# Kernel optimization log

Hardware: AMD Instinct MI355X
Metric: run time of the kernel (lower is better)

Reference implementation:

```python
import jax, jax.numpy as jnp
import numpy as np

N_NODES = 100000


def gcn_conv(x, edge_index, W, b, n_nodes):
    # PyG GCNConv: add self-loops, symmetric normalization D^-1/2 (A+I) D^-1/2, then XW + b
    xw = x @ W  # [N, out]
    loops = jnp.arange(n_nodes, dtype=edge_index.dtype)
    src = jnp.concatenate([edge_index[0], loops])  # [E+N]
    dst = jnp.concatenate([edge_index[1], loops])
    deg = jax.ops.segment_sum(jnp.ones_like(dst, dtype=xw.dtype), dst, num_segments=n_nodes)
    dinv = jnp.where(deg > 0, deg ** -0.5, 0.0).astype(xw.dtype)
    norm = dinv[src] * dinv[dst]  # [E+N]
    msgs = xw[src] * norm[:, None]  # gather source features, scale
    out = jax.ops.segment_sum(msgs, dst, num_segments=n_nodes)  # scatter-add at dst
    return out + b


def setup_inputs() -> dict:
    key = jax.random.key(0)
    k1, k2, k3, k4 = jax.random.split(key, 4)
    F_in, dim, n_cls, n_edges = 512, 32, 40, 3200000
    x = jax.random.normal(k1, (N_NODES, F_in), dtype=jnp.float32)
    edge_index = jax.random.randint(k2, (2, n_edges), 0, N_NODES, dtype=jnp.int64)
    W1 = jax.random.normal(k3, (F_in, dim), dtype=jnp.float32) * (1.0 / np.sqrt(F_in))
    b1 = jnp.zeros((dim,), dtype=jnp.float32)
    W2 = jax.random.normal(k4, (dim, n_cls), dtype=jnp.float32) * (1.0 / np.sqrt(dim))
    b2 = jnp.zeros((n_cls,), dtype=jnp.float32)
    return {"x": x, "edge_index": edge_index, "W1": W1, "b1": b1, "W2": W2, "b2": b2}


def reference(x, edge_index, W1, b1, W2, b2):
    h = jax.nn.relu(gcn_conv(x, edge_index, W1, b1, N_NODES))
    # F.dropout with training=False (eval) is identity
    logits = gcn_conv(h, edge_index, W2, b2, N_NODES)
    return jax.nn.log_softmax(logits, axis=1)
```

## Files before the change

kernel.cpp:

```cpp
#include <hip/hip_runtime.h>
#include <math.h>


#define DIM 32
#define NCLS 40
#define F_IN 512
#define BSH 8
#define EPB 8192
#define LMAX 9216

__device__ __forceinline__ unsigned int bf16rne(float x) {
    unsigned int u = __float_as_uint(x);
    return (u + 0x7fffu + ((u >> 16) & 1u)) >> 16;
}
__device__ __forceinline__ unsigned int packpair(float lo, float hi) {
    return bf16rne(lo) | (bf16rne(hi) << 16);
}
__device__ __forceinline__ void unpack8(uint4 u, float* f) {
    f[0] = __uint_as_float(u.x << 16);
    f[1] = __uint_as_float(u.x & 0xffff0000u);
    f[2] = __uint_as_float(u.y << 16);
    f[3] = __uint_as_float(u.y & 0xffff0000u);
    f[4] = __uint_as_float(u.z << 16);
    f[5] = __uint_as_float(u.z & 0xffff0000u);
    f[6] = __uint_as_float(u.w << 16);
    f[7] = __uint_as_float(u.w & 0xffff0000u);
}

__global__ __launch_bounds__(256) void initcur_k(int* __restrict__ gcur) {
    int t = blockIdx.x * 256 + threadIdx.x;
    if (t < 512) gcur[t] = t * LMAX;
}

__global__ __launch_bounds__(256) void part_k(const int* __restrict__ src,
                                              const int* __restrict__ dst,
                                              int* __restrict__ gcur,
                                              int* __restrict__ pairs, int E) {
    __shared__ int st[EPB];
    __shared__ int h[512];
    __shared__ int hb[512];
    int tid = threadIdx.x;
    h[tid] = 0; h[tid + 256] = 0;
    __syncthreads();
    int base = blockIdx.x * EPB;
#pragma unroll 4
    for (int k = 0; k < EPB / 256; ++k) {
        int e = base + k * 256 + tid;
        if (e < E) {
            int d = dst[e];
            st[k * 256 + tid] = d;
            atomicAdd(&h[d >> BSH], 1);
        }
    }
    __syncthreads();
    for (int b = tid; b < 512; b += 256) {
        int cnt = h[b];
        hb[b] = cnt ? atomicAdd(&gcur[b], cnt) : 0;
        h[b] = 0;
    }
    __syncthreads();
#pragma unroll 4
    for (int k = 0; k < EPB / 256; ++k) {
        int e = base + k * 256 + tid;
        if (e < E) {
            int d = st[k * 256 + tid];
            int b = d >> BSH;
            int r = atomicAdd(&h[b], 1);
            pairs[hb[b] + r] = ((d & 255) << 17) | src[e];
        }
    }
}

__global__ __launch_bounds__(256) void build_k(const int* __restrict__ pairs,
                                               const int* __restrict__ gcur,
                                               int* __restrict__ rowptr,
                                               int* __restrict__ rowcnt,
                                               int* __restrict__ csr,
                                               float* __restrict__ dinv,
                                               int n) {
    __shared__ int lcsr[LMAX];
    __shared__ int bins[256 * 17];
    __shared__ int cnt[256];
    __shared__ int sc[256];
    __shared__ int cur[256];
    int tid = threadIdx.x;
    int b = blockIdx.x;
    int lo = b * LMAX;
    int cb = gcur[b] - lo;
    if (cb > LMAX) cb = LMAX;
    cnt[tid] = 0;
    __syncthreads();
    const int* Pb = pairs + lo;
    for (int i = tid; i < cb; i += 256)
        atomicAdd(&cnt[Pb[i] >> 17], 1);
    __syncthreads();
    int c = cnt[tid];
    sc[tid] = c;
    __syncthreads();
    for (int off = 1; off < 256; off <<= 1) {
        int v = sc[tid];
        if (tid >= off) v += sc[tid - off];
        __syncthreads();
        sc[tid] = v;
        __syncthreads();
    }
    int excl = sc[tid] - c;
    int v = (b << BSH) + tid;
    if (v < n) {
        rowptr[v] = lo + excl;
        rowcnt[v] = c;
        dinv[v] = rsqrtf((float)(c + 1));
    }
    cur[tid] = excl;
    __syncthreads();
    for (int i = tid; i < cb; i += 256) {
        int p = Pb[i];
        int pos = atomicAdd(&cur[p >> 17], 1);
        lcsr[pos] = p & 0x1FFFF;
    }
    __syncthreads();
    {
        int* mb = &bins[tid * 17];
        int s = excl, e = excl + c;
#pragma unroll
        for (int k = 0; k < 16; ++k) mb[k] = 0;
        for (int i = s; i < e; ++i) ++mb[lcsr[i] >> 13];
        int run = s;
#pragma unroll
        for (int k = 0; k < 16; ++k) { int q = mb[k]; mb[k] = run; run += q; }
        for (int i = s; i < e; ++i) {
            int val = lcsr[i];
            int k = val >> 13;
            int pos = mb[k]++;
            csr[lo + pos] = val;
        }
    }
}

#define GR 128
__global__ __launch_bounds__(256) void gemm1_k(const float* __restrict__ x,
                                               const float* __restrict__ W1,
                                               const float* __restrict__ dinv,
                                               unsigned short* __restrict__ xwp, int n) {
    __shared__ float xs[32 * GR];
    __shared__ float ws[32 * 32];
    int tid = threadIdx.x;
    int base = blockIdx.x * GR;
    int rg = tid & 31;
    int cg = tid >> 5;
    float acc[4][4];
#pragma unroll
    for (int i = 0; i < 4; ++i)
#pragma unroll
        for (int j = 0; j < 4; ++j) acc[i][j] = 0.f;

    int lr = tid >> 1;
    int lq = tid & 1;
    int grow = base + lr;
    if (grow >= n) grow = n - 1;
    const float* xrow = x + (size_t)grow * F_IN;
    int wk = tid >> 3;
    int wc = tid & 7;

    for (int k0 = 0; k0 < F_IN; k0 += 32) {
        float4 a[4];
#pragma unroll
        for (int j = 0; j < 4; ++j)
            a[j] = *(const float4*)(xrow + k0 + lq * 16 + j * 4);
        float4 wv = *(const float4*)(W1 + (size_t)(k0 + wk) * DIM + wc * 4);
        __syncthreads();
#pragma unroll
        for (int j = 0; j < 4; ++j) {
            xs[(lq * 16 + j * 4 + 0) * GR + lr] = a[j].x;
            xs[(lq * 16 + j * 4 + 1) * GR + lr] = a[j].y;
            xs[(lq * 16 + j * 4 + 2) * GR + lr] = a[j].z;
            xs[(lq * 16 + j * 4 + 3) * GR + lr] = a[j].w;
        }
        *(float4*)&ws[wk * 32 + wc * 4] = wv;
        __syncthreads();
#pragma unroll 8
        for (int kk = 0; kk < 32; ++kk) {
            float4 xv = *(const float4*)&xs[kk * GR + rg * 4];
            float4 wv2 = *(const float4*)&ws[kk * 32 + cg * 4];
            acc[0][0] = fmaf(xv.x, wv2.x, acc[0][0]);
            acc[0][1] = fmaf(xv.x, wv2.y, acc[0][1]);
            acc[0][2] = fmaf(xv.x, wv2.z, acc[0][2]);
            acc[0][3] = fmaf(xv.x, wv2.w, acc[0][3]);
            acc[1][0] = fmaf(xv.y, wv2.x, acc[1][0]);
            acc[1][1] = fmaf(xv.y, wv2.y, acc[1][1]);
            acc[1][2] = fmaf(xv.y, wv2.z, acc[1][2]);
            acc[1][3] = fmaf(xv.y, wv2.w, acc[1][3]);
            acc[2][0] = fmaf(xv.z, wv2.x, acc[2][0]);
            acc[2][1] = fmaf(xv.z, wv2.y, acc[2][1]);
            acc[2][2] = fmaf(xv.z, wv2.z, acc[2][2]);
            acc[2][3] = fmaf(xv.z, wv2.w, acc[2][3]);
            acc[3][0] = fmaf(xv.w, wv2.x, acc[3][0]);
            acc[3][1] = fmaf(xv.w, wv2.y, acc[3][1]);
            acc[3][2] = fmaf(xv.w, wv2.z, acc[3][2]);
            acc[3][3] = fmaf(xv.w, wv2.w, acc[3][3]);
        }
    }
#pragma unroll
    for (int i = 0; i < 4; ++i) {
        int row = base + rg * 4 + i;
        if (row < n) {
            float dv = dinv[row];
            uint2 o;
            o.x = packpair(acc[i][0] * dv, acc[i][1] * dv);
            o.y = packpair(acc[i][2] * dv, acc[i][3] * dv);
            *(uint2*)(xwp + (size_t)row * DIM + cg * 4) = o;
        }
    }
}

__device__ __forceinline__ void gather_accum(const uint4* __restrict__ F,
                                             const int* __restrict__ csr,
                                             int e, int end, int f8, float* s) {
    float tmp[8];
    for (; e + 7 < end; e += 8) {
        uint4 a0 = F[(size_t)csr[e]     * 4 + f8];
        uint4 a1 = F[(size_t)csr[e + 1] * 4 + f8];
        uint4 a2 = F[(size_t)csr[e + 2] * 4 + f8];
        uint4 a3 = F[(size_t)csr[e + 3] * 4 + f8];
        uint4 a4 = F[(size_t)csr[e + 4] * 4 + f8];
        uint4 a5 = F[(size_t)csr[e + 5] * 4 + f8];
        uint4 a6 = F[(size_t)csr[e + 6] * 4 + f8];
        uint4 a7 = F[(size_t)csr[e + 7] * 4 + f8];
        unpack8(a0, tmp);
#pragma unroll
        for (int j = 0; j < 8; ++j) s[j] += tmp[j];
        unpack8(a1, tmp);
#pragma unroll
        for (int j = 0; j < 8; ++j) s[j] += tmp[j];
        unpack8(a2, tmp);
#pragma unroll
        for (int j = 0; j < 8; ++j) s[j] += tmp[j];
        unpack8(a3, tmp);
#pragma unroll
        for (int j = 0; j < 8; ++j) s[j] += tmp[j];
        unpack8(a4, tmp);
#pragma unroll
        for (int j = 0; j < 8; ++j) s[j] += tmp[j];
        unpack8(a5, tmp);
#pragma unroll
        for (int j = 0; j < 8; ++j) s[j] += tmp[j];
        unpack8(a6, tmp);
#pragma unroll
        for (int j = 0; j < 8; ++j) s[j] += tmp[j];
        unpack8(a7, tmp);
#pragma unroll
        for (int j = 0; j < 8; ++j) s[j] += tmp[j];
    }
    for (; e + 3 < end; e += 4) {
        uint4 a0 = F[(size_t)csr[e]     * 4 + f8];
        uint4 a1 = F[(size_t)csr[e + 1] * 4 + f8];
        uint4 a2 = F[(size_t)csr[e + 2] * 4 + f8];
        uint4 a3 = F[(size_t)csr[e + 3] * 4 + f8];
        unpack8(a0, tmp);
#pragma unroll
        for (int j = 0; j < 8; ++j) s[j] += tmp[j];
        unpack8(a1, tmp);
#pragma unroll
        for (int j = 0; j < 8; ++j) s[j] += tmp[j];
        unpack8(a2, tmp);
#pragma unroll
        for (int j = 0; j < 8; ++j) s[j] += tmp[j];
        unpack8(a3, tmp);
#pragma unroll
        for (int j = 0; j < 8; ++j) s[j] += tmp[j];
    }
    for (; e < end; ++e) {
        unpack8(F[(size_t)csr[e] * 4 + f8], tmp);
#pragma unroll
        for (int j = 0; j < 8; ++j) s[j] += tmp[j];
    }
}

__global__ __launch_bounds__(256) void agg1_k(const uint4* __restrict__ F,
                                              const int* __restrict__ rowptr,
                                              const int* __restrict__ rowcnt,
                                              const int* __restrict__ csr,
                                              const float* __restrict__ dinv,
                                              const float* __restrict__ bias,
                                              uint4* __restrict__ out, int n) {
    int t = blockIdx.x * 256 + threadIdx.x;
    int v = t >> 2;
    int f8 = t & 3;
    if (v >= n) return;
    float s[8];
    unpack8(F[(size_t)v * 4 + f8], s);
    int e = rowptr[v];
    gather_accum(F, csr, e, e + rowcnt[v], f8, s);
    float dv = dinv[v];
    float4 b0 = *(const float4*)(bias + f8 * 8);
    float4 b1 = *(const float4*)(bias + f8 * 8 + 4);
    float bb[8] = {b0.x, b0.y, b0.z, b0.w, b1.x, b1.y, b1.z, b1.w};
    float r[8];
#pragma unroll
    for (int j = 0; j < 8; ++j) r[j] = fmaxf(s[j] * dv + bb[j], 0.f) * dv;
    uint4 o;
    o.x = packpair(r[0], r[1]);
    o.y = packpair(r[2], r[3]);
    o.z = packpair(r[4], r[5]);
    o.w = packpair(r[6], r[7]);
    out[(size_t)v * 4 + f8] = o;
}

__global__ __launch_bounds__(256) void agg2final_k(const uint4* __restrict__ F,
                                                   const int* __restrict__ rowptr,
                                                   const int* __restrict__ rowcnt,
                                                   const int* __restrict__ csr,
                                                   const float* __restrict__ dinv,
                                                   const float* __restrict__ W2,
                                                   const float* __restrict__ b2,
                                                   float* __restrict__ out, int n) {
    __shared__ float w2s[DIM * NCLS];
    __shared__ float b2s[NCLS];
    __shared__ float a2s[64 * 33];
    int tid = threadIdx.x;
    for (int i = tid; i < DIM * NCLS; i += 256) w2s[i] = W2[i];
    if (tid < NCLS) b2s[tid] = b2[tid];

    int nl = tid >> 2;
    int f8 = tid & 3;
    int v = blockIdx.x * 64 + nl;
    if (v < n) {
        float s[8];
        unpack8(F[(size_t)v * 4 + f8], s);
        int e = rowptr[v];
        gather_accum(F, csr, e, e + rowcnt[v], f8, s);
        float dv = dinv[v];
#pragma unroll
        for (int j = 0; j < 8; ++j) a2s[nl * 33 + f8 * 8 + j] = s[j] * dv;
    }
    __syncthreads();

    int q = f8;
    float lg[10];
#pragma unroll
    for (int c = 0; c < 10; ++c) lg[c] = b2s[q * 10 + c];
#pragma unroll
    for (int k = 0; k < DIM; ++k) {
        float a = a2s[nl * 33 + k];
        const float* wr = &w2s[k * NCLS + q * 10];
#pragma unroll
        for (int c = 0; c < 10; ++c) lg[c] += a * wr[c];
    }
    float m = lg[0];
#pragma unroll
    for (int c = 1; c < 10; ++c) m = fmaxf(m, lg[c]);
    m = fmaxf(m, __shfl_xor(m, 1));
    m = fmaxf(m, __shfl_xor(m, 2));
    float ssum = 0.f;
#pragma unroll
    for (int c = 0; c < 10; ++c) ssum += __expf(lg[c] - m);
    ssum += __shfl_xor(ssum, 1);
    ssum += __shfl_xor(ssum, 2);
    float lse = m + __logf(ssum);
    if (v < n) {
        float* o = out + (size_t)v * NCLS + q * 10;
#pragma unroll
        for (int c = 0; c < 10; ++c) o[c] = lg[c] - lse;
    }
}

extern "C" void kernel_launch(void* const* d_in, const int* in_sizes, int n_in,
                              void* d_out, int out_size, void* d_ws, size_t ws_size,
                              hipStream_t stream) {
    const float* x  = (const float*)d_in[0];
    const int*   ei = (const int*)d_in[1];
    const float* W1 = (const float*)d_in[2];
    const float* b1 = (const float*)d_in[3];
    const float* W2 = (const float*)d_in[4];
    const float* b2 = (const float*)d_in[5];
    float* out = (float*)d_out;

    int n = in_sizes[0] / F_IN;
    int E = in_sizes[1] / 2;
    const int* src = ei;
    const int* dst = ei + E;
    int nbk = (n + 255) >> BSH;
    size_t padE = (size_t)nbk * LMAX;

    char* w = (char*)d_ws;
    size_t off = 0;
    auto alloc = [&](size_t bytes) -> void* {
        void* p = w + off;
        off += (bytes + 255) & ~(size_t)255;
        return p;
    };
    size_t featB2 = ((size_t)n * DIM * 2 + 255) & ~(size_t)255;
    int*   csr    = (int*)alloc(padE * 4);
    char*  pairsR = (char*)alloc(padE * 4);
    int*   rowptr = (int*)alloc((size_t)n * 4);
    int*   rowcnt = (int*)alloc((size_t)n * 4);
    float* dinv   = (float*)alloc((size_t)n * 4);
    int*   gcur   = (int*)alloc(512 * 4);
    (void)ws_size;

    int*            pairs = (int*)pairsR;
    unsigned short* xwp   = (unsigned short*)pairsR;
    unsigned short* hts   = (unsigned short*)(pairsR + featB2);

    int nebk = (E + EPB - 1) / EPB;
    initcur_k<<<2, 256, 0, stream>>>(gcur);
    part_k <<<nebk, 256, 0, stream>>>(src, dst, gcur, pairs, E);
    build_k<<<nbk, 256, 0, stream>>>(pairs, gcur, rowptr, rowcnt, csr, dinv, n);

    gemm1_k<<<(n + GR - 1) / GR, 256, 0, stream>>>(x, W1, dinv, xwp, n);
    agg1_k<<<((size_t)n * 4 + 255) / 256, 256, 0, stream>>>(
        (const uint4*)xwp, rowptr, rowcnt, csr, dinv, b1, (uint4*)hts, n);
    agg2final_k<<<(n + 63) / 64, 256, 0, stream>>>(
        (const uint4*)hts, rowptr, rowcnt, csr, dinv, W2, b2, out, n);
}
```

Measured before the change: 496.7 us.

## Split GEMM1 K dimension across two blocks with atomic accumulation and separate pack

The first GEMM now launches two blocks per 128-row tile, each covering half of the 512-wide K dimension. Partial results are accumulated into a zeroed fp32 buffer with atomicAdd. A new pack kernel then applies the dinv scaling and converts to bf16. This doubles the block count to raise parallelism and latency hiding for the GEMM. In exchange it adds a memset, fp32 atomic traffic, and an extra kernel pass over the intermediate buffer.

```diff
diff --git a/kernel.cpp b/kernel.cpp
--- a/kernel.cpp
+++ b/kernel.cpp
@@ -140,12 +140,13 @@
 #define GR 128
 __global__ __launch_bounds__(256) void gemm1_k(const float* __restrict__ x,
                                                const float* __restrict__ W1,
-                                               const float* __restrict__ dinv,
-                                               unsigned short* __restrict__ xwp, int n) {
+                                               float* __restrict__ xwf, int n) {
     __shared__ float xs[32 * GR];
     __shared__ float ws[32 * 32];
     int tid = threadIdx.x;
-    int base = blockIdx.x * GR;
+    int tile = blockIdx.x >> 1;
+    int kh = blockIdx.x & 1;
+    int base = tile * GR;
     int rg = tid & 31;
     int cg = tid >> 5;
     float acc[4][4];
@@ -162,7 +163,8 @@
     int wk = tid >> 3;
     int wc = tid & 7;
 
-    for (int k0 = 0; k0 < F_IN; k0 += 32) {
+    int kbeg = kh * 256, kend = kbeg + 256;
+    for (int k0 = kbeg; k0 < kend; k0 += 32) {
         float4 a[4];
 #pragma unroll
         for (int j = 0; j < 4; ++j)
@@ -204,13 +206,29 @@
     for (int i = 0; i < 4; ++i) {
         int row = base + rg * 4 + i;
         if (row < n) {
-            float dv = dinv[row];
-            uint2 o;
-            o.x = packpair(acc[i][0] * dv, acc[i][1] * dv);
-            o.y = packpair(acc[i][2] * dv, acc[i][3] * dv);
-            *(uint2*)(xwp + (size_t)row * DIM + cg * 4) = o;
-        }
-    }
+            float* o = xwf + (size_t)row * DIM + cg * 4;
+#pragma unroll
+            for (int j = 0; j < 4; ++j) atomicAdd(&o[j], acc[i][j]);
+        }
+    }
+}
+
+__global__ __launch_bounds__(256) void pack_k(const float* __restrict__ xwf,
+                                              const float* __restrict__ dinv,
+                                              unsigned short* __restrict__ xwp, int n) {
+    int t = blockIdx.x * 256 + threadIdx.x;
+    int v = t >> 2;
+    int f8 = t & 3;
+    if (v >= n) return;
+    const float4* p = (const float4*)(xwf + (size_t)v * DIM + f8 * 8);
+    float4 p0 = p[0], p1 = p[1];
+    float dv = dinv[v];
+    uint4 o;
+    o.x = packpair(p0.x * dv, p0.y * dv);
+    o.y = packpair(p0.z * dv, p0.w * dv);
+    o.z = packpair(p1.x * dv, p1.y * dv);
+    o.w = packpair(p1.z * dv, p1.w * dv);
+    *(uint4*)(xwp + (size_t)v * DIM + f8 * 8) = o;
 }
 
 __device__ __forceinline__ void gather_accum(const uint4* __restrict__ F,
@@ -396,6 +414,7 @@
     int*   rowcnt = (int*)alloc((size_t)n * 4);
     float* dinv   = (float*)alloc((size_t)n * 4);
     int*   gcur   = (int*)alloc(512 * 4);
+    float* xwf    = (float*)alloc((size_t)n * DIM * 4);
     (void)ws_size;
 
     int*            pairs = (int*)pairsR;
@@ -403,11 +422,15 @@
     unsigned short* hts   = (unsigned short*)(pairsR + featB2);
 
     int nebk = (E + EPB - 1) / EPB;
+    int ntile = (n + GR - 1) / GR;
+
+    hipMemsetAsync(xwf, 0, (size_t)n * DIM * 4, stream);
     initcur_k<<<2, 256, 0, stream>>>(gcur);
     part_k <<<nebk, 256, 0, stream>>>(src, dst, gcur, pairs, E);
     build_k<<<nbk, 256, 0, stream>>>(pairs, gcur, rowptr, rowcnt, csr, dinv, n);
 
-    gemm1_k<<<(n + GR - 1) / GR, 256, 0, stream>>>(x, W1, dinv, xwp, n);
+    gemm1_k<<<ntile * 2, 256, 0, stream>>>(x, W1, xwf, n);
+    pack_k <<<((size_t)n * 4 + 255) / 256, 256, 0, stream>>>(xwf, dinv, xwp, n);
     agg1_k<<<((size_t)n * 4 + 255) / 256, 256, 0, stream>>>(
         (const uint4*)xwp, rowptr, rowcnt, csr, dinv, b1, (uint4*)hts, n);
     agg2final_k<<<(n + 63) / 64, 256, 0, stream>>>(
```

Result: slower. 628.2 us (+26.5%).
